# Optimization experiments

Hardware: AMD Instinct MI355X
Metric: run time of the kernel (lower is better)

## Reference

```python
import jax, jax.numpy as jnp
import numpy as np

BLOCK_SIZE = 256
NEG = -10000.0  # matches the module's additive mask constant (not -inf)

def setup_inputs() -> dict:
    key = jax.random.key(0)
    qkv = jax.random.normal(key, (4, 4096, 192), dtype=jnp.float32)
    return {"qkv": qkv}

def reference(qkv):
    B, S, dm = qkv.shape
    d = dm // 3
    q, k, v = qkv[..., :d], qkv[..., d:2*d], qkv[..., 2*d:]
    scale = 1.0 / jnp.sqrt(jnp.asarray(d, dtype=qkv.dtype))
    scores = jnp.einsum('bqd,bkd->bqk', q, k * scale)  # [B,S,S]
    i = jnp.arange(S)[:, None]
    j = jnp.arange(S)[None, :]
    # allowed: i - block_size <= j <= i ; else additive -10000 (as in torch code)
    mask = jnp.where((j <= i) & (j >= i - BLOCK_SIZE), 0.0, NEG).astype(scores.dtype)
    attn = jax.nn.softmax(scores + mask[None, :, :], axis=-1)
    return jnp.einsum('bqk,bkd->bqd', attn, v)
```

## Files before the change

kernel.cpp:

```cpp
#include <hip/hip_runtime.h>
#include <hip/hip_bf16.h>


#define LOG2E 1.4426950408889634f

typedef __attribute__((ext_vector_type(8))) short  frag;
typedef __attribute__((ext_vector_type(4))) float  f32x4;

static __device__ inline short f2bf(float x) {
    __hip_bfloat16 h = __float2bfloat16(x);
    return __builtin_bit_cast(short, h);
}

#define DPPF(x, ctrl) __builtin_bit_cast(float, \
    __builtin_amdgcn_mov_dpp(__builtin_bit_cast(int, (x)), (ctrl), 0xF, 0xF, true))

static __device__ inline float red16_max(float x) {
    x = fmaxf(x, DPPF(x, 0xB1));
    x = fmaxf(x, DPPF(x, 0x4E));
    x = fmaxf(x, DPPF(x, 0x141));
    x = fmaxf(x, DPPF(x, 0x140));
    return x;
}
static __device__ inline float red16_sum(float x) {
    x += DPPF(x, 0xB1);
    x += DPPF(x, 0x4E);
    x += DPPF(x, 0x141);
    x += DPPF(x, 0x140);
    return x;
}

#define LSTR 72
#define PSTR 40
#define OSTR 65

__global__ __launch_bounds__(512, 2) void swa_mfma2(const float* __restrict__ qkv,
                                                    float* __restrict__ out)
{
    __shared__ short Qs[64 * LSTR];
    __shared__ short Ks[64 * LSTR];
    __shared__ short Vt[64 * LSTR];
    __shared__ short Pw[8][16 * PSTR];
    __shared__ float Om[4][16 * OSTR];
    __shared__ float2 mlbuf[4][16];

    const int b    = blockIdx.y;
    const int q0   = blockIdx.x * 64;
    const int t    = threadIdx.x;
    const int w    = t >> 6;
    const int s    = w & 3;
    const int g    = w >> 2;
    const int lane = t & 63;
    const int cl   = lane & 15;
    const int quad = lane >> 4;
    const int ql   = 4 * quad;

    const float4* qkv4 = (const float4*)qkv;
    const int r_st = t >> 3;
    const int c8   = t & 7;

    {
        const size_t base = (size_t)(b * 4096 + q0 + r_st) * 48;
        #pragma unroll
        for (int i = 0; i < 2; ++i) {
            float4 v = qkv4[base + c8 + 8 * i];
            short4 s4 = { f2bf(v.x * 0.125f), f2bf(v.y * 0.125f),
                          f2bf(v.z * 0.125f), f2bf(v.w * 0.125f) };
            *(short4*)&Qs[r_st * LSTR + 4 * (c8 + 8 * i)] = s4;
        }
    }

    const int c0 = (q0 >= 256) ? 0 : (4 - (q0 >> 6));

    float4 preK[2], preV[2];
    {
        const int kb = q0 - 256 + 64 * c0;
        const size_t base = (size_t)(b * 4096 + kb + r_st) * 48;
        #pragma unroll
        for (int i = 0; i < 2; ++i) {
            preK[i] = qkv4[base + 16 + c8 + 8 * i];
            preV[i] = qkv4[base + 32 + c8 + 8 * i];
        }
    }

    __syncthreads();
    const frag qf0 = *(const frag*)&Qs[(16 * s + cl) * LSTR + 8 * quad];
    const frag qf1 = *(const frag*)&Qs[(16 * s + cl) * LSTR + 32 + 8 * quad];

    float m[4], l[4];
    f32x4 oacc[4];
    #pragma unroll
    for (int r = 0; r < 4; ++r) { m[r] = -1e30f; l[r] = 0.f; }
    #pragma unroll
    for (int n4 = 0; n4 < 4; ++n4) oacc[n4] = (f32x4){0.f, 0.f, 0.f, 0.f};

    for (int c = c0; c < 5; ++c) {
        __syncthreads();

        #pragma unroll
        for (int i = 0; i < 2; ++i) {
            short4 k4 = { f2bf(preK[i].x), f2bf(preK[i].y),
                          f2bf(preK[i].z), f2bf(preK[i].w) };
            *(short4*)&Ks[r_st * LSTR + 4 * (c8 + 8 * i)] = k4;
            const int d0 = 4 * (c8 + 8 * i);
            Vt[(d0 + 0) * LSTR + r_st] = f2bf(preV[i].x);
            Vt[(d0 + 1) * LSTR + r_st] = f2bf(preV[i].y);
            Vt[(d0 + 2) * LSTR + r_st] = f2bf(preV[i].z);
            Vt[(d0 + 3) * LSTR + r_st] = f2bf(preV[i].w);
        }
        __syncthreads();

        if (c < 4) {
            const int kb = q0 - 256 + 64 * (c + 1);
            const size_t base = (size_t)(b * 4096 + kb + r_st) * 48;
            #pragma unroll
            for (int i = 0; i < 2; ++i) {
                preK[i] = qkv4[base + 16 + c8 + 8 * i];
                preV[i] = qkv4[base + 32 + c8 + 8 * i];
            }
        }

        f32x4 sc[2];
        #pragma unroll
        for (int u = 0; u < 2; ++u) {
            const int t4 = 2 * g + u;
            sc[u] = (f32x4){0.f, 0.f, 0.f, 0.f};
            const frag kf0 = *(const frag*)&Ks[(16 * t4 + cl) * LSTR + 8 * quad];
            const frag kf1 = *(const frag*)&Ks[(16 * t4 + cl) * LSTR + 32 + 8 * quad];
            sc[u] = __builtin_amdgcn_mfma_f32_16x16x32_bf16(qf0, kf0, sc[u], 0, 0, 0);
            sc[u] = __builtin_amdgcn_mfma_f32_16x16x32_bf16(qf1, kf1, sc[u], 0, 0, 0);
        }

        if (c == 4) {
            #pragma unroll
            for (int u = 0; u < 2; ++u) {
                const int t4 = 2 * g + u;
                #pragma unroll
                for (int r = 0; r < 4; ++r)
                    if (16 * s + ql + r < 16 * t4 + cl) sc[u][r] = -1e30f;
            }
        } else if (c == 0) {
            #pragma unroll
            for (int u = 0; u < 2; ++u) {
                const int t4 = 2 * g + u;
                #pragma unroll
                for (int r = 0; r < 4; ++r)
                    if (16 * s + ql + r > 16 * t4 + cl) sc[u][r] = -1e30f;
            }
        }

        #pragma unroll
        for (int r = 0; r < 4; ++r) {
            float mx = red16_max(fmaxf(sc[0][r], sc[1][r]));
            const float mnew  = fmaxf(m[r], mx);
            const float alpha = __builtin_amdgcn_exp2f((m[r] - mnew) * LOG2E);
            m[r] = mnew;
            float sum = 0.f;
            #pragma unroll
            for (int u = 0; u < 2; ++u) {
                float p = (sc[u][r] <= -1e29f)
                            ? 0.f
                            : __builtin_amdgcn_exp2f((sc[u][r] - mnew) * LOG2E);
                Pw[w][(ql + r) * PSTR + 16 * u + cl] = f2bf(p);
                sum += p;
            }
            l[r] = l[r] * alpha + red16_sum(sum);
            #pragma unroll
            for (int n4 = 0; n4 < 4; ++n4) oacc[n4][r] *= alpha;
        }

        const frag pf = *(const frag*)&Pw[w][cl * PSTR + 8 * quad];
        #pragma unroll
        for (int n4 = 0; n4 < 4; ++n4) {
            const frag vf = *(const frag*)&Vt[(16 * n4 + cl) * LSTR + 32 * g + 8 * quad];
            oacc[n4] = __builtin_amdgcn_mfma_f32_16x16x32_bf16(pf, vf, oacc[n4], 0, 0, 0);
        }
    }

    if (g == 1) {
        #pragma unroll
        for (int n4 = 0; n4 < 4; ++n4)
            #pragma unroll
            for (int r = 0; r < 4; ++r)
                Om[s][(ql + r) * OSTR + 16 * n4 + cl] = oacc[n4][r];
        if (cl == 0)
            #pragma unroll
            for (int r = 0; r < 4; ++r)
                mlbuf[s][ql + r] = make_float2(m[r], l[r]);
    }
    __syncthreads();
    if (g == 0) {
        #pragma unroll
        for (int r = 0; r < 4; ++r) {
            const float2 ml1 = mlbuf[s][ql + r];
            const float M  = fmaxf(m[r], ml1.x);
            const float a0 = __builtin_amdgcn_exp2f((m[r]  - M) * LOG2E);
            const float a1 = __builtin_amdgcn_exp2f((ml1.x - M) * LOG2E);
            const float L  = l[r] * a0 + ml1.y * a1;
            const float inv = 1.0f / L;
            const size_t row = (size_t)(b * 4096 + q0 + 16 * s + ql + r) * 64;
            #pragma unroll
            for (int n4 = 0; n4 < 4; ++n4) {
                const float o1 = Om[s][(ql + r) * OSTR + 16 * n4 + cl];
                out[row + 16 * n4 + cl] = (oacc[n4][r] * a0 + o1 * a1) * inv;
            }
        }
    }
}

extern "C" void kernel_launch(void* const* d_in, const int* in_sizes, int n_in,
                              void* d_out, int out_size, void* d_ws, size_t ws_size,
                              hipStream_t stream) {
    const float* qkv = (const float*)d_in[0];
    float* out = (float*)d_out;
    dim3 grid(64, 4);
    dim3 block(512);
    hipLaunchKernelGGL(swa_mfma2, grid, block, 0, stream, qkv, out);
}
```

Before: 67.60 us.

## Stage all five K/V chunks into shared memory upfront, load Q directly to registers

Measured after the change: 72.75 us. 1.08x slower.

```diff
diff --git a/kernel.cpp b/kernel.cpp
--- a/kernel.cpp
+++ b/kernel.cpp
@@ -10,6 +10,15 @@
 static __device__ inline short f2bf(float x) {
     __hip_bfloat16 h = __float2bfloat16(x);
     return __builtin_bit_cast(short, h);
+}
+
+static __device__ inline frag cvt8(float4 a, float4 b, float sc) {
+    frag f;
+    f[0] = f2bf(a.x * sc); f[1] = f2bf(a.y * sc);
+    f[2] = f2bf(a.z * sc); f[3] = f2bf(a.w * sc);
+    f[4] = f2bf(b.x * sc); f[5] = f2bf(b.y * sc);
+    f[6] = f2bf(b.z * sc); f[7] = f2bf(b.w * sc);
+    return f;
 }
 
 #define DPPF(x, ctrl) __builtin_bit_cast(float, \
@@ -30,16 +39,16 @@
     return x;
 }
 
-#define LSTR 72
+#define KSTR 72
+#define VSTR 328
 #define PSTR 40
 #define OSTR 65
 
-__global__ __launch_bounds__(512, 2) void swa_mfma2(const float* __restrict__ qkv,
+__global__ __launch_bounds__(512, 2) void swa_mfma3(const float* __restrict__ qkv,
                                                     float* __restrict__ out)
 {
-    __shared__ short Qs[64 * LSTR];
-    __shared__ short Ks[64 * LSTR];
-    __shared__ short Vt[64 * LSTR];
+    __shared__ short Ks[320 * KSTR];
+    __shared__ short Vt[64 * VSTR];
     __shared__ short Pw[8][16 * PSTR];
     __shared__ float Om[4][16 * OSTR];
     __shared__ float2 mlbuf[4][16];
@@ -56,36 +65,45 @@
     const int ql   = 4 * quad;
 
     const float4* qkv4 = (const float4*)qkv;
-    const int r_st = t >> 3;
-    const int c8   = t & 7;
-
+    const int c0 = (q0 >= 256) ? 0 : (4 - (q0 >> 6));
+
+    float4 kA[5], kB[5], vA[5], vB[5];
+    #pragma unroll
+    for (int c = 0; c < 5; ++c) {
+        int kb = q0 - 256 + 64 * c; if (kb < 0) kb = 0;
+        const size_t base = (size_t)(b * 4096 + kb + lane) * 48 + 2 * w;
+        kA[c] = qkv4[base + 16];
+        kB[c] = qkv4[base + 17];
+        vA[c] = qkv4[base + 32];
+        vB[c] = qkv4[base + 33];
+    }
+
+    frag qf0, qf1;
     {
-        const size_t base = (size_t)(b * 4096 + q0 + r_st) * 48;
-        #pragma unroll
-        for (int i = 0; i < 2; ++i) {
-            float4 v = qkv4[base + c8 + 8 * i];
-            short4 s4 = { f2bf(v.x * 0.125f), f2bf(v.y * 0.125f),
-                          f2bf(v.z * 0.125f), f2bf(v.w * 0.125f) };
-            *(short4*)&Qs[r_st * LSTR + 4 * (c8 + 8 * i)] = s4;
-        }
-    }
-
-    const int c0 = (q0 >= 256) ? 0 : (4 - (q0 >> 6));
-
-    float4 preK[2], preV[2];
-    {
-        const int kb = q0 - 256 + 64 * c0;
-        const size_t base = (size_t)(b * 4096 + kb + r_st) * 48;
-        #pragma unroll
-        for (int i = 0; i < 2; ++i) {
-            preK[i] = qkv4[base + 16 + c8 + 8 * i];
-            preV[i] = qkv4[base + 32 + c8 + 8 * i];
-        }
-    }
-
+        const size_t qrow = (size_t)(b * 4096 + q0 + 16 * s + cl) * 48;
+        float4 qa = qkv4[qrow + 2 * quad];
+        float4 qb = qkv4[qrow + 2 * quad + 1];
+        float4 qc = qkv4[qrow + 8 + 2 * quad];
+        float4 qd = qkv4[qrow + 8 + 2 * quad + 1];
+        qf0 = cvt8(qa, qb, 0.125f);
+        qf1 = cvt8(qc, qd, 0.125f);
+    }
+
+    #pragma unroll
+    for (int c = 0; c < 5; ++c) {
+        *(frag*)&Ks[(64 * c + lane) * KSTR + 8 * w] = cvt8(kA[c], kB[c], 1.0f);
+        const int col = 64 * c + lane;
+        const int d0  = 8 * w;
+        Vt[(d0 + 0) * VSTR + col] = f2bf(vA[c].x);
+        Vt[(d0 + 1) * VSTR + col] = f2bf(vA[c].y);
+        Vt[(d0 + 2) * VSTR + col] = f2bf(vA[c].z);
+        Vt[(d0 + 3) * VSTR + col] = f2bf(vA[c].w);
+        Vt[(d0 + 4) * VSTR + col] = f2bf(vB[c].x);
+        Vt[(d0 + 5) * VSTR + col] = f2bf(vB[c].y);
+        Vt[(d0 + 6) * VSTR + col] = f2bf(vB[c].z);
+        Vt[(d0 + 7) * VSTR + col] = f2bf(vB[c].w);
+    }
     __syncthreads();
-    const frag qf0 = *(const frag*)&Qs[(16 * s + cl) * LSTR + 8 * quad];
-    const frag qf1 = *(const frag*)&Qs[(16 * s + cl) * LSTR + 32 + 8 * quad];
 
     float m[4], l[4];
     f32x4 oacc[4];
@@ -95,38 +113,13 @@
     for (int n4 = 0; n4 < 4; ++n4) oacc[n4] = (f32x4){0.f, 0.f, 0.f, 0.f};
 
     for (int c = c0; c < 5; ++c) {
-        __syncthreads();
-
-        #pragma unroll
-        for (int i = 0; i < 2; ++i) {
-            short4 k4 = { f2bf(preK[i].x), f2bf(preK[i].y),
-                          f2bf(preK[i].z), f2bf(preK[i].w) };
-            *(short4*)&Ks[r_st * LSTR + 4 * (c8 + 8 * i)] = k4;
-            const int d0 = 4 * (c8 + 8 * i);
-            Vt[(d0 + 0) * LSTR + r_st] = f2bf(preV[i].x);
-            Vt[(d0 + 1) * LSTR + r_st] = f2bf(preV[i].y);
-            Vt[(d0 + 2) * LSTR + r_st] = f2bf(preV[i].z);
-            Vt[(d0 + 3) * LSTR + r_st] = f2bf(preV[i].w);
-        }
-        __syncthreads();
-
-        if (c < 4) {
-            const int kb = q0 - 256 + 64 * (c + 1);
-            const size_t base = (size_t)(b * 4096 + kb + r_st) * 48;
-            #pragma unroll
-            for (int i = 0; i < 2; ++i) {
-                preK[i] = qkv4[base + 16 + c8 + 8 * i];
-                preV[i] = qkv4[base + 32 + c8 + 8 * i];
-            }
-        }
-
         f32x4 sc[2];
         #pragma unroll
         for (int u = 0; u < 2; ++u) {
-            const int t4 = 2 * g + u;
+            const int row = 64 * c + 16 * (2 * g + u) + cl;
             sc[u] = (f32x4){0.f, 0.f, 0.f, 0.f};
-            const frag kf0 = *(const frag*)&Ks[(16 * t4 + cl) * LSTR + 8 * quad];
-            const frag kf1 = *(const frag*)&Ks[(16 * t4 + cl) * LSTR + 32 + 8 * quad];
+            const frag kf0 = *(const frag*)&Ks[row * KSTR + 8 * quad];
+            const frag kf1 = *(const frag*)&Ks[row * KSTR + 32 + 8 * quad];
             sc[u] = __builtin_amdgcn_mfma_f32_16x16x32_bf16(qf0, kf0, sc[u], 0, 0, 0);
             sc[u] = __builtin_amdgcn_mfma_f32_16x16x32_bf16(qf1, kf1, sc[u], 0, 0, 0);
         }
@@ -172,7 +165,8 @@
         const frag pf = *(const frag*)&Pw[w][cl * PSTR + 8 * quad];
         #pragma unroll
         for (int n4 = 0; n4 < 4; ++n4) {
-            const frag vf = *(const frag*)&Vt[(16 * n4 + cl) * LSTR + 32 * g + 8 * quad];
+            const frag vf = *(const frag*)&Vt[(16 * n4 + cl) * VSTR
+                                              + 64 * c + 32 * g + 8 * quad];
             oacc[n4] = __builtin_amdgcn_mfma_f32_16x16x32_bf16(pf, vf, oacc[n4], 0, 0, 0);
         }
     }
@@ -215,5 +209,5 @@
     float* out = (float*)d_out;
     dim3 grid(64, 4);
     dim3 block(512);
-    hipLaunchKernelGGL(swa_mfma2, grid, block, 0, stream, qkv, out);
-}
+    hipLaunchKernelGGL(swa_mfma3, grid, block, 0, stream, qkv, out);
+}
```
